# Kernel tuning notes

Measured on AMD Instinct MI355X. Metric: run time of the kernel, lower is better.

The kernel has to match this reference:

```python
import jax, jax.numpy as jnp
import numpy as np

ALPHA = 0.2  # LeakyReLU negative slope
NEG_INF = -9e15


def make_quaternion_mul(kernel):
    # kernel: (in/4, out); returns hamilton: (in, out)
    r, i, j, k = jnp.split(kernel, 4, axis=1)
    r2 = jnp.concatenate([r, -i, -j, -k], axis=0)
    i2 = jnp.concatenate([i, r, -k, j], axis=0)
    j2 = jnp.concatenate([j, k, r, -i], axis=0)
    k2 = jnp.concatenate([k, -j, i, r], axis=0)
    return jnp.concatenate([r2, i2, j2, k2], axis=1)


def setup_inputs() -> dict:
    key = jax.random.key(0)
    k1, k2, k3, k4 = jax.random.split(key, 4)
    N, IN, OUT, H = 4096, 512, 128, 4
    x = jax.random.normal(k1, (N, IN), dtype=jnp.float32)
    adj = jax.random.randint(k2, (N, N), 0, 2, dtype=jnp.int32)
    stdv = float(np.sqrt(6.0 / (IN // 4 + OUT)))
    W = jax.random.uniform(k3, (H, IN // 4, OUT), dtype=jnp.float32,
                           minval=-stdv, maxval=stdv)
    a_std = float(np.sqrt(2.0 / (2 * OUT + 1))) * 1.414
    a = jax.random.normal(k4, (H, 2 * OUT), dtype=jnp.float32) * a_std
    return {"x": x, "adj": adj, "W": W, "a": a}


def reference(x, adj, W, a):
    N = x.shape[0]
    hamilton = jax.vmap(make_quaternion_mul)(W)          # (H, IN, OUT)
    h = jnp.einsum('nf,hfo->hno', x, hamilton)           # (H, N, OUT)
    OUT = h.shape[-1]
    a_src, a_dst = a[:, :OUT], a[:, OUT:]
    # e[h,i,j] = leakyrelu(h_i . a_src + h_j . a_dst), same math as repeat/cat
    f_src = jnp.einsum('hno,ho->hn', h, a_src)           # (H, N)
    f_dst = jnp.einsum('hno,ho->hn', h, a_dst)           # (H, N)
    e = jax.nn.leaky_relu(f_src[:, :, None] + f_dst[:, None, :], ALPHA)
    e = jnp.where((adj > 0)[None, :, :], e, NEG_INF)
    attn = jax.nn.softmax(e, axis=-1)                    # (H, N, N)
    # dropout p=0.0 / eval mode -> identity
    h_prime = jnp.einsum('hnm,hmo->hno', attn, h)        # (H, N, OUT)
    out = jnp.transpose(h_prime, (1, 0, 2)).reshape(N, -1)  # concat heads
    return jax.nn.elu(out)
```

## Files before the change

### kernel.cpp

```cpp
#include <hip/hip_runtime.h>
#include <math.h>

#define ALPHA 0.2f

#define XS   544
#define HS   4128
#define HCS  66048

typedef __attribute__((ext_vector_type(8))) short short8;
typedef __attribute__((ext_vector_type(4))) float f32x4;
typedef __attribute__((ext_vector_type(4))) int i32x4;

__device__ __forceinline__ unsigned short f2bf(float f) {
    unsigned int x = __float_as_uint(f);
    x += 0x7fffu + ((x >> 16) & 1u);
    return (unsigned short)(x >> 16);
}
__device__ __forceinline__ unsigned int pack_rne(float lo, float hi) {
    return (unsigned int)f2bf(lo) | ((unsigned int)f2bf(hi) << 16);
}
__device__ __forceinline__ unsigned int pack_trunc(float lo, float hi) {
    return __builtin_amdgcn_perm(__float_as_uint(hi), __float_as_uint(lo), 0x07060302u);
}
__device__ __forceinline__ unsigned int bitmask1(unsigned int x, int j) {
    return (unsigned int)(((int)(x << (31 - j))) >> 31);
}

__global__ __launch_bounds__(256) void k_prep(const float* __restrict__ x,
                                              const float* __restrict__ W,
                                              const int* __restrict__ adj,
                                              unsigned short* __restrict__ xbf,
                                              unsigned short* __restrict__ hamT,
                                              unsigned int* __restrict__ adjp32) {
    const int b = blockIdx.x;
    if (b < 1024) {
        const int gid = b * 256 + threadIdx.x;
        const int row = gid >> 6, c8 = (gid & 63) * 8;
        const float4* xp = (const float4*)x + (size_t)gid * 2;
        const float4 f0 = xp[0], f1 = xp[1];
        const uint4 o = {pack_rne(f0.x, f0.y), pack_rne(f0.z, f0.w),
                         pack_rne(f1.x, f1.y), pack_rne(f1.z, f1.w)};
        *(uint4*)(xbf + (size_t)row * XS + c8) = o;
    } else if (b < 1152) {
        const int gid = (b - 1024) * 256 + threadIdx.x;
        const int head = gid >> 13;
        const int rem  = gid & 8191;
        const int o = rem >> 6, f8 = rem & 63;
        const int ob = o >> 5, oc = o & 31;
        float v[8];
#pragma unroll
        for (int j = 0; j < 8; j++) {
            const int f = f8 * 8 + j;
            const int bq = f >> 7, f0 = f & 127;
            const float s = ((0x5390u >> ((bq << 2) | ob)) & 1u) ? -1.0f : 1.0f;
            v[j] = s * W[(head << 14) + (f0 << 7) + (((bq ^ ob) << 5) | oc)];
        }
        const uint4 pk = {pack_rne(v[0], v[1]), pack_rne(v[2], v[3]),
                          pack_rne(v[4], v[5]), pack_rne(v[6], v[7])};
        *(uint4*)(hamT + (size_t)(head * 128 + o) * XS + f8 * 8) = pk;
    } else {
        const int gid = (b - 1152) * 256 + threadIdx.x;
        const int4* ap = (const int4*)(adj + (size_t)gid * 32);
        unsigned int u = 0;
#pragma unroll
        for (int q = 0; q < 8; q++) {
            const int4 v = ap[q];
            u |= (v.x > 0 ? 1u : 0u) << (q * 4);
            u |= (v.y > 0 ? 2u : 0u) << (q * 4);
            u |= (v.z > 0 ? 4u : 0u) << (q * 4);
            u |= (v.w > 0 ? 8u : 0u) << (q * 4);
        }
        adjp32[gid] = u;
    }
}

__global__ __launch_bounds__(256) void k_h(const unsigned short* __restrict__ xbf,
                                           const unsigned short* __restrict__ hamT,
                                           const float* __restrict__ a,
                                           unsigned short* __restrict__ hBT,
                                           float2* __restrict__ fsE,
                                           float2* __restrict__ fdE) {
    const int t = threadIdx.x;
    const int head = blockIdx.y;
    const int n0 = blockIdx.x * 64;
    const int wv = t >> 6, lane = t & 63;
    const int quad = lane >> 4, nl = lane & 15;
    const unsigned short* ap = xbf + (size_t)(n0 + wv * 16 + nl) * XS + quad * 8;
    const unsigned short* bp = hamT + (size_t)(head * 128 + nl) * XS + quad * 8;
    f32x4 acc[8];
#pragma unroll
    for (int ct = 0; ct < 8; ct++) acc[ct] = (f32x4){0.f, 0.f, 0.f, 0.f};
    for (int kc = 0; kc < 16; kc++) {
        const short8 af = *(const short8*)(ap + kc * 32);
#pragma unroll
        for (int ct = 0; ct < 8; ct++) {
            const short8 bf_ = *(const short8*)(bp + (size_t)ct * 16 * XS + kc * 32);
            acc[ct] = __builtin_amdgcn_mfma_f32_16x16x32_bf16(af, bf_, acc[ct], 0, 0, 0);
        }
    }
    const int rbase = n0 + wv * 16 + quad * 4;
#pragma unroll
    for (int ct = 0; ct < 8; ct++) {
        const uint2 pk = {pack_rne(acc[ct][0], acc[ct][1]), pack_rne(acc[ct][2], acc[ct][3])};
        *(uint2*)(hBT + (size_t)(head * 128 + ct * 16 + nl) * HS + rbase) = pk;
    }
    float fsr[4] = {0.f, 0.f, 0.f, 0.f}, fdr[4] = {0.f, 0.f, 0.f, 0.f};
#pragma unroll
    for (int ct = 0; ct < 8; ct++) {
        const int col = ct * 16 + nl;
        const float as = a[head * 256 + col];
        const float ad = a[head * 256 + 128 + col];
#pragma unroll
        for (int r = 0; r < 4; r++) {
            fsr[r] += acc[ct][r] * as;
            fdr[r] += acc[ct][r] * ad;
        }
    }
#pragma unroll
    for (int off = 1; off < 16; off <<= 1)
#pragma unroll
        for (int r = 0; r < 4; r++) {
            fsr[r] += __shfl_xor(fsr[r], off, 64);
            fdr[r] += __shfl_xor(fdr[r], off, 64);
        }
    if (nl == 0) {
#pragma unroll
        for (int r = 0; r < 4; r++) {
            const int n = rbase + r;
            fsE[(head << 12) + n] = make_float2(__expf(fsr[r]), __expf(ALPHA * fsr[r]));
            fdE[(head << 12) + n] = make_float2(__expf(fdr[r]), __expf(ALPHA * fdr[r]));
        }
    }
}

#define WELT(e1, ea, j, bits, es) \
    __uint_as_float(__float_as_uint(fmaxf((es).x * (e1), (es).y * (ea))) & bitmask1((bits), (j)))
#define WPK(f4, jb, bits, es) \
    pack_trunc(WELT((f4).x, (f4).y, (jb), (bits), (es)), \
               WELT((f4).z, (f4).w, (jb) + 1, (bits), (es)))
#define BLOAD(ct, moff) (*(const short8*)(bbase + (size_t)(ct) * HCS + (moff)))

#define STAGE_LOAD(P, mcn) do {                                           \
    const int _mo = (mcn) * 32;                                           \
    P##b0 = BLOAD(0, _mo); P##b1 = BLOAD(1, _mo);                         \
    P##b2 = BLOAD(2, _mo); P##b3 = BLOAD(3, _mo);                         \
    P##b4 = BLOAD(4, _mo); P##b5 = BLOAD(5, _mo);                         \
    P##b6 = BLOAD(6, _mo); P##b7 = BLOAD(7, _mo);                         \
    P##k0 = ap0[(mcn) * 4]; P##k1 = ap1[(mcn) * 4];                       \
    P##f0 = fdb[(mcn) * 16];     P##f1 = fdb[(mcn) * 16 + 1];             \
    P##f2 = fdb[(mcn) * 16 + 2]; P##f3 = fdb[(mcn) * 16 + 3];             \
} while (0)

#define STAGE_EXEC(P) do {                                                \
    const i32x4 _a0 = {(int)WPK(P##f0, 0, P##k0, es0), (int)WPK(P##f1, 2, P##k0, es0), \
                       (int)WPK(P##f2, 4, P##k0, es0), (int)WPK(P##f3, 6, P##k0, es0)}; \
    const i32x4 _a1 = {(int)WPK(P##f0, 0, P##k1, es1), (int)WPK(P##f1, 2, P##k1, es1), \
                       (int)WPK(P##f2, 4, P##k1, es1), (int)WPK(P##f3, 6, P##k1, es1)}; \
    const short8 _af0 = __builtin_bit_cast(short8, _a0);                  \
    const short8 _af1 = __builtin_bit_cast(short8, _a1);                  \
    acc[0][0] = __builtin_amdgcn_mfma_f32_16x16x32_bf16(_af0, P##b0, acc[0][0], 0, 0, 0); \
    acc[1][0] = __builtin_amdgcn_mfma_f32_16x16x32_bf16(_af1, P##b0, acc[1][0], 0, 0, 0); \
    acc[0][1] = __builtin_amdgcn_mfma_f32_16x16x32_bf16(_af0, P##b1, acc[0][1], 0, 0, 0); \
    acc[1][1] = __builtin_amdgcn_mfma_f32_16x16x32_bf16(_af1, P##b1, acc[1][1], 0, 0, 0); \
    acc[0][2] = __builtin_amdgcn_mfma_f32_16x16x32_bf16(_af0, P##b2, acc[0][2], 0, 0, 0); \
    acc[1][2] = __builtin_amdgcn_mfma_f32_16x16x32_bf16(_af1, P##b2, acc[1][2], 0, 0, 0); \
    acc[0][3] = __builtin_amdgcn_mfma_f32_16x16x32_bf16(_af0, P##b3, acc[0][3], 0, 0, 0); \
    acc[1][3] = __builtin_amdgcn_mfma_f32_16x16x32_bf16(_af1, P##b3, acc[1][3], 0, 0, 0); \
    acc[0][4] = __builtin_amdgcn_mfma_f32_16x16x32_bf16(_af0, P##b4, acc[0][4], 0, 0, 0); \
    acc[1][4] = __builtin_amdgcn_mfma_f32_16x16x32_bf16(_af1, P##b4, acc[1][4], 0, 0, 0); \
    acc[0][5] = __builtin_amdgcn_mfma_f32_16x16x32_bf16(_af0, P##b5, acc[0][5], 0, 0, 0); \
    acc[1][5] = __builtin_amdgcn_mfma_f32_16x16x32_bf16(_af1, P##b5, acc[1][5], 0, 0, 0); \
    acc[0][6] = __builtin_amdgcn_mfma_f32_16x16x32_bf16(_af0, P##b6, acc[0][6], 0, 0, 0); \
    acc[1][6] = __builtin_amdgcn_mfma_f32_16x16x32_bf16(_af1, P##b6, acc[1][6], 0, 0, 0); \
    acc[0][7] = __builtin_amdgcn_mfma_f32_16x16x32_bf16(_af0, P##b7, acc[0][7], 0, 0, 0); \
    acc[1][7] = __builtin_amdgcn_mfma_f32_16x16x32_bf16(_af1, P##b7, acc[1][7], 0, 0, 0); \
    accL0 = __builtin_amdgcn_mfma_f32_16x16x32_bf16(_af0, ones, accL0, 0, 0, 0); \
    accL1 = __builtin_amdgcn_mfma_f32_16x16x32_bf16(_af1, ones, accL1, 0, 0, 0); \
} while (0)

__global__ __launch_bounds__(256, 2) void k_attn(const unsigned char* __restrict__ adjp,
                                                 const float2* __restrict__ fsE,
                                                 const float2* __restrict__ fdE,
                                                 const unsigned short* __restrict__ hBT,
                                                 float* __restrict__ out) {
    __shared__ f32x4 cbuf[3584];
    const int t = threadIdx.x;
    const int head = blockIdx.x & 3;
    const int n0 = (blockIdx.x >> 2) * 32;
    const int wv = t >> 6, lane = t & 63;
    const int quad = lane >> 4, nl = lane & 15;
    const int m0base = wv << 10;
    const float2 es0 = fsE[(head << 12) + n0 + nl];
    const float2 es1 = fsE[(head << 12) + n0 + 16 + nl];
    const unsigned char* ap0 = adjp + ((size_t)(n0 + nl) << 9) + (m0base >> 3) + quad;
    const unsigned char* ap1 = ap0 + (16u << 9);
    const float4* fdb = (const float4*)(fdE + (head << 12) + m0base + quad * 8);
    const unsigned short* bbase = hBT + (size_t)(head * 128 + nl) * HS + quad * 8 + m0base;
    const short8 ones = __builtin_bit_cast(short8,
        (i32x4){0x3F803F80, 0x3F803F80, 0x3F803F80, 0x3F803F80});
    f32x4 acc[2][8];
    f32x4 accL0 = (f32x4){0.f, 0.f, 0.f, 0.f}, accL1 = (f32x4){0.f, 0.f, 0.f, 0.f};
#pragma unroll
    for (int rt = 0; rt < 2; rt++)
#pragma unroll
        for (int ct = 0; ct < 8; ct++) acc[rt][ct] = (f32x4){0.f, 0.f, 0.f, 0.f};
    short8 Ab0, Ab1, Ab2, Ab3, Ab4, Ab5, Ab6, Ab7;
    short8 Bb0, Bb1, Bb2, Bb3, Bb4, Bb5, Bb6, Bb7;
    unsigned int Ak0, Ak1, Bk0, Bk1;
    float4 Af0, Af1, Af2, Af3, Bf0, Bf1, Bf2, Bf3;
    STAGE_LOAD(A, 0);
    STAGE_LOAD(B, 1);
    for (int mc = 0; mc < 32; mc += 2) {
        STAGE_EXEC(A);
        STAGE_LOAD(A, (mc + 2) & 31);
        STAGE_EXEC(B);
        STAGE_LOAD(B, (mc + 3) & 31);
    }
#pragma unroll
    for (int rt = 0; rt < 2; rt++)
#pragma unroll
        for (int ct = 0; ct < 8; ct++) {
            const int owner = ct & 3;
            if (owner != wv) {
                const int j = (wv - owner - 1) & 3;
                cbuf[((rt * 8 + ct) * 3 + j) * 64 + lane] = acc[rt][ct];
            }
        }
    cbuf[3072 + wv * 64 + lane] = accL0;
    cbuf[3072 + (4 + wv) * 64 + lane] = accL1;
    __syncthreads();
#pragma unroll
    for (int rt = 0; rt < 2; rt++) {
        f32x4 Lt = (f32x4){0.f, 0.f, 0.f, 0.f};
#pragma unroll
        for (int v = 0; v < 4; v++) Lt += cbuf[3072 + (rt * 4 + v) * 64 + lane];
        float iL[4];
#pragma unroll
        for (int r = 0; r < 4; r++) iL[r] = (Lt[r] > 0.f) ? (1.0f / Lt[r]) : 0.0f;
#pragma unroll
        for (int ct = 0; ct < 8; ct++) {
            if ((ct & 3) == wv) {
                f32x4 tot = acc[rt][ct];
#pragma unroll
                for (int j = 0; j < 3; j++) tot += cbuf[((rt * 8 + ct) * 3 + j) * 64 + lane];
#pragma unroll
                for (int r = 0; r < 4; r++) {
                    float v = tot[r] * iL[r];
                    v = v > 0.f ? v : (__expf(v) - 1.0f);
                    out[(size_t)(n0 + rt * 16 + quad * 4 + r) * 512
                        + head * 128 + ct * 16 + nl] = v;
                }
            }
        }
    }
}

extern "C" void kernel_launch(void* const* d_in, const int* in_sizes, int n_in,
                              void* d_out, int out_size, void* d_ws, size_t ws_size,
                              hipStream_t stream) {
    (void)in_sizes; (void)n_in; (void)out_size; (void)ws_size;
    const float* x   = (const float*)d_in[0];
    const int*   adj = (const int*)d_in[1];
    const float* W   = (const float*)d_in[2];
    const float* a   = (const float*)d_in[3];
    float* out = (float*)d_out;

    char* ws = (char*)d_ws;
    unsigned short* xbf  = (unsigned short*)(ws);
    unsigned short* hBT  = (unsigned short*)(ws + 4456448);
    unsigned short* hamT = (unsigned short*)(ws + 8683520);
    unsigned char*  adjp = (unsigned char*)(ws + 9240576);
    float2*         fsE  = (float2*)(ws + 11337728);
    float2*         fdE  = (float2*)(ws + 11468800);

    hipLaunchKernelGGL(k_prep, dim3(3200),    dim3(256), 0, stream,
                       x, W, adj, xbf, hamT, (unsigned int*)adjp);
    hipLaunchKernelGGL(k_h,    dim3(64, 4),   dim3(256), 0, stream, xbf, hamT, a, hBT, fsE, fdE);
    hipLaunchKernelGGL(k_attn, dim3(512),     dim3(256), 0, stream, adjp, fsE, fdE, hBT, out);
}
```

Baseline: 176.8 us.

## Double row tile per attention block to reuse B fragments across 64 rows

Each attention block now covers 64 query rows (four 16-row tiles) instead of 32, so every loaded h fragment feeds twice as many MFMAs and global B traffic is halved. The grid drops to 256 blocks with launch bounds of one block per SM, and the cross-wave reduction is processed one row tile at a time through a smaller shared buffer plus a separate buffer for the row sums. The cost is much higher register pressure (128 accumulator vectors), lower occupancy, and only 256 blocks, which may underfill the 256 CUs.

```diff
diff --git a/kernel.cpp b/kernel.cpp
--- a/kernel.cpp
+++ b/kernel.cpp
@@ -138,102 +138,98 @@
 #define WPK(f4, jb, bits, es) \
     pack_trunc(WELT((f4).x, (f4).y, (jb), (bits), (es)), \
                WELT((f4).z, (f4).w, (jb) + 1, (bits), (es)))
-#define BLOAD(ct, moff) (*(const short8*)(bbase + (size_t)(ct) * HCS + (moff)))
-
-#define STAGE_LOAD(P, mcn) do {                                           \
+
+#define LOADM(S, mcn) do {                                                \
     const int _mo = (mcn) * 32;                                           \
-    P##b0 = BLOAD(0, _mo); P##b1 = BLOAD(1, _mo);                         \
-    P##b2 = BLOAD(2, _mo); P##b3 = BLOAD(3, _mo);                         \
-    P##b4 = BLOAD(4, _mo); P##b5 = BLOAD(5, _mo);                         \
-    P##b6 = BLOAD(6, _mo); P##b7 = BLOAD(7, _mo);                         \
-    P##k0 = ap0[(mcn) * 4]; P##k1 = ap1[(mcn) * 4];                       \
-    P##f0 = fdb[(mcn) * 16];     P##f1 = fdb[(mcn) * 16 + 1];             \
-    P##f2 = fdb[(mcn) * 16 + 2]; P##f3 = fdb[(mcn) * 16 + 3];             \
+    _Pragma("unroll")                                                     \
+    for (int _ct = 0; _ct < 8; _ct++)                                     \
+        Bst[S][_ct] = *(const short8*)(bbase + (size_t)_ct * HCS + _mo);  \
+    _Pragma("unroll")                                                     \
+    for (int _rt = 0; _rt < 4; _rt++) Kst[S][_rt] = ap[_rt][(mcn) * 4];   \
+    _Pragma("unroll")                                                     \
+    for (int _q = 0; _q < 4; _q++) Fst[S][_q] = fdb[(mcn) * 16 + _q];     \
 } while (0)
 
-#define STAGE_EXEC(P) do {                                                \
-    const i32x4 _a0 = {(int)WPK(P##f0, 0, P##k0, es0), (int)WPK(P##f1, 2, P##k0, es0), \
-                       (int)WPK(P##f2, 4, P##k0, es0), (int)WPK(P##f3, 6, P##k0, es0)}; \
-    const i32x4 _a1 = {(int)WPK(P##f0, 0, P##k1, es1), (int)WPK(P##f1, 2, P##k1, es1), \
-                       (int)WPK(P##f2, 4, P##k1, es1), (int)WPK(P##f3, 6, P##k1, es1)}; \
-    const short8 _af0 = __builtin_bit_cast(short8, _a0);                  \
-    const short8 _af1 = __builtin_bit_cast(short8, _a1);                  \
-    acc[0][0] = __builtin_amdgcn_mfma_f32_16x16x32_bf16(_af0, P##b0, acc[0][0], 0, 0, 0); \
-    acc[1][0] = __builtin_amdgcn_mfma_f32_16x16x32_bf16(_af1, P##b0, acc[1][0], 0, 0, 0); \
-    acc[0][1] = __builtin_amdgcn_mfma_f32_16x16x32_bf16(_af0, P##b1, acc[0][1], 0, 0, 0); \
-    acc[1][1] = __builtin_amdgcn_mfma_f32_16x16x32_bf16(_af1, P##b1, acc[1][1], 0, 0, 0); \
-    acc[0][2] = __builtin_amdgcn_mfma_f32_16x16x32_bf16(_af0, P##b2, acc[0][2], 0, 0, 0); \
-    acc[1][2] = __builtin_amdgcn_mfma_f32_16x16x32_bf16(_af1, P##b2, acc[1][2], 0, 0, 0); \
-    acc[0][3] = __builtin_amdgcn_mfma_f32_16x16x32_bf16(_af0, P##b3, acc[0][3], 0, 0, 0); \
-    acc[1][3] = __builtin_amdgcn_mfma_f32_16x16x32_bf16(_af1, P##b3, acc[1][3], 0, 0, 0); \
-    acc[0][4] = __builtin_amdgcn_mfma_f32_16x16x32_bf16(_af0, P##b4, acc[0][4], 0, 0, 0); \
-    acc[1][4] = __builtin_amdgcn_mfma_f32_16x16x32_bf16(_af1, P##b4, acc[1][4], 0, 0, 0); \
-    acc[0][5] = __builtin_amdgcn_mfma_f32_16x16x32_bf16(_af0, P##b5, acc[0][5], 0, 0, 0); \
-    acc[1][5] = __builtin_amdgcn_mfma_f32_16x16x32_bf16(_af1, P##b5, acc[1][5], 0, 0, 0); \
-    acc[0][6] = __builtin_amdgcn_mfma_f32_16x16x32_bf16(_af0, P##b6, acc[0][6], 0, 0, 0); \
-    acc[1][6] = __builtin_amdgcn_mfma_f32_16x16x32_bf16(_af1, P##b6, acc[1][6], 0, 0, 0); \
-    acc[0][7] = __builtin_amdgcn_mfma_f32_16x16x32_bf16(_af0, P##b7, acc[0][7], 0, 0, 0); \
-    acc[1][7] = __builtin_amdgcn_mfma_f32_16x16x32_bf16(_af1, P##b7, acc[1][7], 0, 0, 0); \
-    accL0 = __builtin_amdgcn_mfma_f32_16x16x32_bf16(_af0, ones, accL0, 0, 0, 0); \
-    accL1 = __builtin_amdgcn_mfma_f32_16x16x32_bf16(_af1, ones, accL1, 0, 0, 0); \
+#define EXECM(S) do {                                                     \
+    short8 _af[4];                                                        \
+    _Pragma("unroll")                                                     \
+    for (int _rt = 0; _rt < 4; _rt++) {                                   \
+        const i32x4 _ai = {(int)WPK(Fst[S][0], 0, Kst[S][_rt], es[_rt]),  \
+                           (int)WPK(Fst[S][1], 2, Kst[S][_rt], es[_rt]),  \
+                           (int)WPK(Fst[S][2], 4, Kst[S][_rt], es[_rt]),  \
+                           (int)WPK(Fst[S][3], 6, Kst[S][_rt], es[_rt])}; \
+        _af[_rt] = __builtin_bit_cast(short8, _ai);                       \
+    }                                                                     \
+    _Pragma("unroll")                                                     \
+    for (int _rt = 0; _rt < 4; _rt++) {                                   \
+        _Pragma("unroll")                                                 \
+        for (int _ct = 0; _ct < 8; _ct++)                                 \
+            acc[_rt][_ct] = __builtin_amdgcn_mfma_f32_16x16x32_bf16(      \
+                _af[_rt], Bst[S][_ct], acc[_rt][_ct], 0, 0, 0);           \
+        accL[_rt] = __builtin_amdgcn_mfma_f32_16x16x32_bf16(              \
+            _af[_rt], ones, accL[_rt], 0, 0, 0);                          \
+    }                                                                     \
 } while (0)
 
-__global__ __launch_bounds__(256, 2) void k_attn(const unsigned char* __restrict__ adjp,
+__global__ __launch_bounds__(256, 1) void k_attn(const unsigned char* __restrict__ adjp,
                                                  const float2* __restrict__ fsE,
                                                  const float2* __restrict__ fdE,
                                                  const unsigned short* __restrict__ hBT,
                                                  float* __restrict__ out) {
-    __shared__ f32x4 cbuf[3584];
+    __shared__ f32x4 cbuf[1536];
+    __shared__ f32x4 Lbuf[1024];
     const int t = threadIdx.x;
     const int head = blockIdx.x & 3;
-    const int n0 = (blockIdx.x >> 2) * 32;
+    const int n0 = (blockIdx.x >> 2) * 64;
     const int wv = t >> 6, lane = t & 63;
     const int quad = lane >> 4, nl = lane & 15;
     const int m0base = wv << 10;
-    const float2 es0 = fsE[(head << 12) + n0 + nl];
-    const float2 es1 = fsE[(head << 12) + n0 + 16 + nl];
-    const unsigned char* ap0 = adjp + ((size_t)(n0 + nl) << 9) + (m0base >> 3) + quad;
-    const unsigned char* ap1 = ap0 + (16u << 9);
+    float2 es[4];
+    const unsigned char* ap[4];
+#pragma unroll
+    for (int rt = 0; rt < 4; rt++) {
+        es[rt] = fsE[(head << 12) + n0 + rt * 16 + nl];
+        ap[rt] = adjp + ((size_t)(n0 + rt * 16 + nl) << 9) + (m0base >> 3) + quad;
+    }
     const float4* fdb = (const float4*)(fdE + (head << 12) + m0base + quad * 8);
     const unsigned short* bbase = hBT + (size_t)(head * 128 + nl) * HS + quad * 8 + m0base;
     const short8 ones = __builtin_bit_cast(short8,
         (i32x4){0x3F803F80, 0x3F803F80, 0x3F803F80, 0x3F803F80});
-    f32x4 acc[2][8];
-    f32x4 accL0 = (f32x4){0.f, 0.f, 0.f, 0.f}, accL1 = (f32x4){0.f, 0.f, 0.f, 0.f};
-#pragma unroll
-    for (int rt = 0; rt < 2; rt++)
+    f32x4 acc[4][8], accL[4];
+#pragma unroll
+    for (int rt = 0; rt < 4; rt++) {
+        accL[rt] = (f32x4){0.f, 0.f, 0.f, 0.f};
 #pragma unroll
         for (int ct = 0; ct < 8; ct++) acc[rt][ct] = (f32x4){0.f, 0.f, 0.f, 0.f};
-    short8 Ab0, Ab1, Ab2, Ab3, Ab4, Ab5, Ab6, Ab7;
-    short8 Bb0, Bb1, Bb2, Bb3, Bb4, Bb5, Bb6, Bb7;
-    unsigned int Ak0, Ak1, Bk0, Bk1;
-    float4 Af0, Af1, Af2, Af3, Bf0, Bf1, Bf2, Bf3;
-    STAGE_LOAD(A, 0);
-    STAGE_LOAD(B, 1);
+    }
+    short8 Bst[2][8];
+    unsigned int Kst[2][4];
+    float4 Fst[2][4];
+    LOADM(0, 0);
+    LOADM(1, 1);
     for (int mc = 0; mc < 32; mc += 2) {
-        STAGE_EXEC(A);
-        STAGE_LOAD(A, (mc + 2) & 31);
-        STAGE_EXEC(B);
-        STAGE_LOAD(B, (mc + 3) & 31);
-    }
-#pragma unroll
-    for (int rt = 0; rt < 2; rt++)
+        EXECM(0);
+        LOADM(0, (mc + 2) & 31);
+        EXECM(1);
+        LOADM(1, (mc + 3) & 31);
+    }
+#pragma unroll
+    for (int rt = 0; rt < 4; rt++) Lbuf[(wv * 4 + rt) * 64 + lane] = accL[rt];
+#pragma unroll
+    for (int rt = 0; rt < 4; rt++) {
+        if (rt > 0) __syncthreads();
 #pragma unroll
         for (int ct = 0; ct < 8; ct++) {
             const int owner = ct & 3;
             if (owner != wv) {
                 const int j = (wv - owner - 1) & 3;
-                cbuf[((rt * 8 + ct) * 3 + j) * 64 + lane] = acc[rt][ct];
+                cbuf[(ct * 3 + j) * 64 + lane] = acc[rt][ct];
             }
         }
-    cbuf[3072 + wv * 64 + lane] = accL0;
-    cbuf[3072 + (4 + wv) * 64 + lane] = accL1;
-    __syncthreads();
-#pragma unroll
-    for (int rt = 0; rt < 2; rt++) {
+        __syncthreads();
         f32x4 Lt = (f32x4){0.f, 0.f, 0.f, 0.f};
 #pragma unroll
-        for (int v = 0; v < 4; v++) Lt += cbuf[3072 + (rt * 4 + v) * 64 + lane];
+        for (int v = 0; v < 4; v++) Lt += Lbuf[(v * 4 + rt) * 64 + lane];
         float iL[4];
 #pragma unroll
         for (int r = 0; r < 4; r++) iL[r] = (Lt[r] > 0.f) ? (1.0f / Lt[r]) : 0.0f;
@@ -242,7 +238,7 @@
             if ((ct & 3) == wv) {
                 f32x4 tot = acc[rt][ct];
 #pragma unroll
-                for (int j = 0; j < 3; j++) tot += cbuf[((rt * 8 + ct) * 3 + j) * 64 + lane];
+                for (int j = 0; j < 3; j++) tot += cbuf[(ct * 3 + j) * 64 + lane];
 #pragma unroll
                 for (int r = 0; r < 4; r++) {
                     float v = tot[r] * iL[r];
@@ -276,5 +272,5 @@
     hipLaunchKernelGGL(k_prep, dim3(3200),    dim3(256), 0, stream,
                        x, W, adj, xbf, hamT, (unsigned int*)adjp);
     hipLaunchKernelGGL(k_h,    dim3(64, 4),   dim3(256), 0, stream, xbf, hamT, a, hBT, fsE, fdE);
-    hipLaunchKernelGGL(k_attn, dim3(512),     dim3(256), 0, stream, adjp, fsE, fdE, hBT, out);
-}
+    hipLaunchKernelGGL(k_attn, dim3(256),     dim3(256), 0, stream, adjp, fsE, fdE, hBT, out);
+}
```

Result: faster. 160.0 us (-9.5%).
